# Performance work log

Hardware: AMD Instinct MI355X
Metric: run time of the kernel (lower is better)

## Reference

```python
import jax, jax.numpy as jnp
import numpy as np

DIM = 1024
NUM_HEADS = 16
SEQ_LEN = 4096


def setup_inputs() -> dict:
    key = jax.random.key(0)
    ks = jax.random.split(key, 9)
    s = DIM ** -0.5  # typical init scale for weights
    return {
        "x": jax.random.normal(ks[0], (SEQ_LEN, DIM), dtype=jnp.float32),
        "Wq": jax.random.normal(ks[1], (DIM, DIM), dtype=jnp.float32) * s,
        "bq": jax.random.normal(ks[2], (DIM,), dtype=jnp.float32) * s,
        "Wk": jax.random.normal(ks[3], (DIM, DIM), dtype=jnp.float32) * s,
        "bk": jax.random.normal(ks[4], (DIM,), dtype=jnp.float32) * s,
        "Wv": jax.random.normal(ks[5], (DIM, DIM), dtype=jnp.float32) * s,
        "bv": jax.random.normal(ks[6], (DIM,), dtype=jnp.float32) * s,
        "Wp": jax.random.normal(ks[7], (DIM, DIM), dtype=jnp.float32) * s,
        "bp": jax.random.normal(ks[8], (DIM,), dtype=jnp.float32) * s,
    }


def reference(x, Wq, bq, Wk, bk, Wv, bv, Wp, bp):
    T, C = x.shape
    H = NUM_HEADS
    Dh = C // H
    # QKV projections (eqx.nn.Linear: y = W @ x + b, vmapped over tokens)
    q = (x @ Wq.T + bq).reshape(T, H, Dh).swapaxes(0, 1)  # [H, T, Dh]
    k = (x @ Wk.T + bk).reshape(T, H, Dh).swapaxes(0, 1)
    v = (x @ Wv.T + bv).reshape(T, H, Dh).swapaxes(0, 1)
    # NOTE: original scales by C**-0.5 (full dim), not head_dim**-0.5
    attn = jnp.einsum("htd,hsd->hts", q, k) * (C ** -0.5)  # [H, T, T]
    causal = jnp.tril(jnp.ones((T, T), dtype=bool))[None, :, :]
    attn = jnp.where(causal, attn, -jnp.inf)
    attn = jax.nn.softmax(attn, axis=-1)
    out = jnp.einsum("hts,hsd->htd", attn, v)  # [H, T, Dh]
    out = out.swapaxes(0, 1).reshape(T, C)
    return out @ Wp.T + bp
```

## Files before the change

kernel.cpp:

```cpp
#include <hip/hip_runtime.h>
#include <stdint.h>

typedef unsigned short u16;
typedef __bf16 bf16x8 __attribute__((ext_vector_type(8)));
typedef u16 u16x8 __attribute__((ext_vector_type(8)));
typedef u16 u16x4 __attribute__((ext_vector_type(4)));
typedef float f32x4 __attribute__((ext_vector_type(4)));
typedef float f32x16 __attribute__((ext_vector_type(16)));

#define SEQ 4096
#define CD 1024
#define NH 16
#define DHD 64

__device__ __forceinline__ u16 f2bf(float f) {
  union { float f; unsigned u; } v; v.f = f;
  unsigned r = v.u + 0x7fffu + ((v.u >> 16) & 1u);
  return (u16)(r >> 16);
}
__device__ __forceinline__ unsigned fbits(float f) {
  union { float f; unsigned u; } v; v.f = f; return v.u;
}

__device__ __forceinline__ void load_lds16(const u16* g, u16* l) {
  __builtin_amdgcn_global_load_lds((const __attribute__((address_space(1))) void*)g,
                                   (__attribute__((address_space(3))) void*)l, 16, 0, 0);
}

__global__ __launch_bounds__(256) void cvt_all(const float* __restrict__ x, const float* __restrict__ Wq,
                                               const float* __restrict__ Wk, const float* __restrict__ Wv,
                                               const float* __restrict__ Wp,
                                               u16* __restrict__ xb, u16* __restrict__ Wb, u16* __restrict__ Wpb) {
  int b = blockIdx.x;
  const float* src; u16* dst; int base;
  if (b < 2048)      { src = x;  dst = xb;             base = b; }
  else if (b < 2560) { src = Wq; dst = Wb;             base = b - 2048; }
  else if (b < 3072) { src = Wk; dst = Wb + CD * CD;   base = b - 2560; }
  else if (b < 3584) { src = Wv; dst = Wb + 2*CD*CD;   base = b - 3072; }
  else               { src = Wp; dst = Wpb;            base = b - 3584; }
  int i = (base * 256 + (int)threadIdx.x) * 8;
  float4 a = *(const float4*)(src + i);
  float4 c = *(const float4*)(src + i + 4);
  u16x8 o;
  o[0] = f2bf(a.x); o[1] = f2bf(a.y); o[2] = f2bf(a.z); o[3] = f2bf(a.w);
  o[4] = f2bf(c.x); o[5] = f2bf(c.y); o[6] = f2bf(c.z); o[7] = f2bf(c.w);
  *(u16x8*)(dst + i) = o;
}

template<int MODE>
__device__ __forceinline__ void gemm_core(const u16* __restrict__ A, const u16* __restrict__ Bw,
                                          const float* __restrict__ bias, void* __restrict__ outp,
                                          float oscale) {
  constexpr int K = CD, N = CD;
  __shared__ u16 As[128 * 32];
  __shared__ u16 Bs[128 * 32];
  const int tid = threadIdx.x;
  const int w = tid >> 6, L = tid & 63, q = L >> 4, ln = L & 15;
  const int rowA0 = blockIdx.y * 128, rowB0 = blockIdx.x * 128;
  const int wr = (w >> 1) * 64, wc = (w & 1) * 64;
  f32x4 acc[4][4] = {};
  for (int k0 = 0; k0 < K; k0 += 32) {
#pragma unroll
    for (int pass = 0; pass < 2; ++pass) {
      int off = pass * 4096 + tid * 16;
      int row = off >> 6;
      int cole = (off & 63) >> 1;
      load_lds16(A + (size_t)(rowA0 + row) * K + k0 + cole, As + pass * 2048 + w * 512);
      load_lds16(Bw + (size_t)(rowB0 + row) * K + k0 + cole, Bs + pass * 2048 + w * 512);
    }
    __syncthreads();
    bf16x8 af[4], bg[4];
#pragma unroll
    for (int i = 0; i < 4; ++i) af[i] = *(const bf16x8*)(As + (wr + i * 16 + ln) * 32 + q * 8);
#pragma unroll
    for (int i = 0; i < 4; ++i) bg[i] = *(const bf16x8*)(Bs + (wc + i * 16 + ln) * 32 + q * 8);
#pragma unroll
    for (int i = 0; i < 4; ++i)
#pragma unroll
      for (int j = 0; j < 4; ++j)
        acc[i][j] = __builtin_amdgcn_mfma_f32_16x16x32_bf16(af[i], bg[j], acc[i][j], 0, 0, 0);
    __syncthreads();
  }
#pragma unroll
  for (int i = 0; i < 4; ++i) {
#pragma unroll
    for (int j = 0; j < 4; ++j) {
      int col = rowB0 + wc + j * 16 + ln;
      float bb = bias[col];
#pragma unroll
      for (int r = 0; r < 4; ++r) {
        int row = rowA0 + wr + i * 16 + q * 4 + r;
        float v = (acc[i][j][r] + bb) * oscale;
        if (MODE == 0)      ((u16*)outp)[(size_t)row * N + col] = f2bf(v);
        else if (MODE == 1) ((u16*)outp)[(size_t)col * SEQ + row] = f2bf(v);
        else                ((float*)outp)[(size_t)row * N + col] = v;
      }
    }
  }
}

__global__ __launch_bounds__(256) void gemm_qkv(const u16* __restrict__ A, const u16* __restrict__ W3,
                                                const float* __restrict__ bq, const float* __restrict__ bk,
                                                const float* __restrict__ bv, u16* __restrict__ Qb,
                                                u16* __restrict__ Kb, u16* __restrict__ VTb) {
  int z = blockIdx.z;
  if (z == 0)      gemm_core<0>(A, W3,               bq, Qb,  0.03125f);
  else if (z == 1) gemm_core<0>(A, W3 + CD * CD,     bk, Kb,  1.0f);
  else             gemm_core<1>(A, W3 + 2 * CD * CD, bv, VTb, 1.0f);
}

__global__ __launch_bounds__(256) void gemm_proj(const u16* __restrict__ A, const u16* __restrict__ Bw,
                                                 const float* __restrict__ bias, float* __restrict__ out) {
  gemm_core<2>(A, Bw, bias, out, 1.0f);
}

__global__ __launch_bounds__(128) void attn_kernel(const u16* __restrict__ Q, const u16* __restrict__ Kg,
                                                   const u16* __restrict__ VTg, u16* __restrict__ O) {
  __shared__ u16 Ks[2][64 * 72];
  __shared__ u16 Vt[2][64 * 72];
  const int tid = threadIdx.x, w = tid >> 6, L = tid & 63;
  const int ln = L & 31, hh = L >> 5;
  const int b = blockIdx.x;
  const int qt = (SEQ / 64 - 1) - (b >> 4);
  const int h = b & 15;
  const int colH = h * DHD;
  const int qrow0 = qt * 64 + w * 32;
  bf16x8 qf[4];
#pragma unroll
  for (int kk = 0; kk < 4; ++kk)
    qf[kk] = *(const bf16x8*)(Q + (size_t)(qrow0 + ln) * CD + colH + kk * 16 + hh * 8);
  f32x16 oa[2] = {};
  float lsum = 0.f;
  const int srow = tid >> 3, sx = tid & 7;
  u16x8 kr[4], vr[4];
#pragma unroll
  for (int p = 0; p < 4; ++p) {
    kr[p] = *(const u16x8*)(Kg + (size_t)(p * 16 + srow) * CD + colH + sx * 8);
    vr[p] = *(const u16x8*)(VTg + (size_t)(colH + p * 16 + srow) * SEQ + sx * 8);
  }
  for (int jt = 0; jt <= qt; ++jt) {
    const int buf = jt & 1;
    u16* KsB = Ks[buf];
    u16* VtB = Vt[buf];
#pragma unroll
    for (int p = 0; p < 4; ++p) {
      *(u16x8*)(KsB + (p * 16 + srow) * 72 + sx * 8) = kr[p];
      *(u16x8*)(VtB + (p * 16 + srow) * 72 + sx * 8) = vr[p];
    }
    __syncthreads();
    if (jt < qt) {
      const size_t kb2 = (size_t)(jt + 1) * 64;
#pragma unroll
      for (int p = 0; p < 4; ++p) {
        kr[p] = *(const u16x8*)(Kg + (kb2 + p * 16 + srow) * CD + colH + sx * 8);
        vr[p] = *(const u16x8*)(VTg + (size_t)(colH + p * 16 + srow) * SEQ + kb2 + sx * 8);
      }
    }
    const bool diag = (jt == qt);
    unsigned pk[16];
#pragma unroll
    for (int nt = 0; nt < 2; ++nt) {
      f32x16 a = {};
#pragma unroll
      for (int kk = 0; kk < 4; ++kk) {
        bf16x8 kf = *(const bf16x8*)(KsB + (nt * 32 + ln) * 72 + kk * 16 + hh * 8);
        a = __builtin_amdgcn_mfma_f32_32x32x16_bf16(kf, qf[kk], a, 0, 0, 0);
      }
#pragma unroll
      for (int r = 0; r < 16; ++r) {
        float sv = a[r];
        if (diag) {
          const int key_l = nt * 32 + (r & 3) + 8 * (r >> 2) + 4 * hh;
          if (key_l > w * 32 + ln) sv = -1e30f;
        }
        float p = __expf(sv);
        lsum += p;
        a[r] = p;
      }
#pragma unroll
      for (int i = 0; i < 8; ++i)
        pk[nt * 8 + i] = __builtin_amdgcn_perm(fbits(a[2 * i + 1]), fbits(a[2 * i]), 0x07060302);
    }
#pragma unroll
    for (int b0 = 0; b0 < 16; b0 += 4) {
      asm("v_permlane32_swap_b32 %0, %1" : "+v"(pk[b0 + 0]), "+v"(pk[b0 + 2]));
      asm("v_permlane32_swap_b32 %0, %1" : "+v"(pk[b0 + 1]), "+v"(pk[b0 + 3]));
    }
#pragma unroll
    for (int g = 0; g < 2; ++g)
#pragma unroll
      for (int s = 0; s < 4; ++s) {
        bf16x8 vf = *(const bf16x8*)(VtB + (g * 32 + ln) * 72 + s * 16 + hh * 8);
        union { unsigned u[4]; bf16x8 v; } pf;
        pf.u[0] = pk[s * 4 + 0]; pf.u[1] = pk[s * 4 + 1];
        pf.u[2] = pk[s * 4 + 2]; pf.u[3] = pk[s * 4 + 3];
        oa[g] = __builtin_amdgcn_mfma_f32_32x32x16_bf16(vf, pf.v, oa[g], 0, 0, 0);
      }
  }
  lsum += __shfl_xor(lsum, 32, 64);
  const float inv = 1.0f / lsum;
#pragma unroll
  for (int g = 0; g < 2; ++g)
#pragma unroll
    for (int rg = 0; rg < 4; ++rg) {
      u16x4 ov;
#pragma unroll
      for (int i = 0; i < 4; ++i) ov[i] = f2bf(oa[g][rg * 4 + i] * inv);
      *(u16x4*)(O + (size_t)(qrow0 + ln) * CD + colH + g * 32 + 8 * rg + 4 * hh) = ov;
    }
}

extern "C" void kernel_launch(void* const* d_in, const int* in_sizes, int n_in,
                              void* d_out, int out_size, void* d_ws, size_t ws_size,
                              hipStream_t stream) {
  const float* x  = (const float*)d_in[0];
  const float* Wq = (const float*)d_in[1];
  const float* bq = (const float*)d_in[2];
  const float* Wk = (const float*)d_in[3];
  const float* bk = (const float*)d_in[4];
  const float* Wv = (const float*)d_in[5];
  const float* bv = (const float*)d_in[6];
  const float* Wp = (const float*)d_in[7];
  const float* bp = (const float*)d_in[8];

  char* ws = (char*)d_ws;
  u16* xb  = (u16*)(ws);
  u16* Wb  = (u16*)(ws + (8u << 20));
  u16* Wpb = (u16*)(ws + (14u << 20));
  u16* Qb  = (u16*)(ws + (16u << 20));
  u16* Kb  = (u16*)(ws + (24u << 20));
  u16* VTb = (u16*)(ws + (32u << 20));
  u16* Ab  = (u16*)(ws + (40u << 20));

  cvt_all<<<4096, 256, 0, stream>>>(x, Wq, Wk, Wv, Wp, xb, Wb, Wpb);
  gemm_qkv<<<dim3(CD / 128, SEQ / 128, 3), 256, 0, stream>>>(xb, Wb, bq, bk, bv, Qb, Kb, VTb);
  attn_kernel<<<(SEQ / 64) * NH, 128, 0, stream>>>(Qb, Kb, VTb, Ab);
  gemm_proj<<<dim3(CD / 128, SEQ / 128), 256, 0, stream>>>(Ab, Wpb, bp, (float*)d_out);
}
```

Baseline: 223.6 us.

## Split attention key range across two wave pairs and merge partial sums

The attention block grows from 128 to 256 threads. Two wave pairs each process half of the causal key tiles for the same 64 query rows, each with its own LDS buffer, and their partial outputs and row sums are merged through shared memory at the end. This shortens the serial loop for long rows and raises parallelism, at the cost of an extra LDS reduction and more sync points. It also folds log2(e) into the Q scale so the kernel can use a native exp2, adds s_setprio around the MFMA sections, and splits the row sum into four partial accumulators.

```diff
diff --git a/kernel.cpp b/kernel.cpp
--- a/kernel.cpp
+++ b/kernel.cpp
@@ -20,6 +20,13 @@
 }
 __device__ __forceinline__ unsigned fbits(float f) {
   union { float f; unsigned u; } v; v.f = f; return v.u;
+}
+__device__ __forceinline__ float fexp2(float x) {
+#if __has_builtin(__builtin_amdgcn_exp2f)
+  return __builtin_amdgcn_exp2f(x);
+#else
+  return exp2f(x);
+#endif
 }
 
 __device__ __forceinline__ void load_lds16(const u16* g, u16* l) {
@@ -104,7 +111,7 @@
                                                 const float* __restrict__ bv, u16* __restrict__ Qb,
                                                 u16* __restrict__ Kb, u16* __restrict__ VTb) {
   int z = blockIdx.z;
-  if (z == 0)      gemm_core<0>(A, W3,               bq, Qb,  0.03125f);
+  if (z == 0)      gemm_core<0>(A, W3,               bq, Qb,  0.0450842200f);
   else if (z == 1) gemm_core<0>(A, W3 + CD * CD,     bk, Kb,  1.0f);
   else             gemm_core<1>(A, W3 + 2 * CD * CD, bv, VTb, 1.0f);
 }
@@ -114,100 +121,138 @@
   gemm_core<2>(A, Bw, bias, out, 1.0f);
 }
 
-__global__ __launch_bounds__(128) void attn_kernel(const u16* __restrict__ Q, const u16* __restrict__ Kg,
-                                                   const u16* __restrict__ VTg, u16* __restrict__ O) {
+__global__ __launch_bounds__(256, 4) void attn_kernel(const u16* __restrict__ Q, const u16* __restrict__ Kg,
+                                                      const u16* __restrict__ VTg, u16* __restrict__ O) {
   __shared__ u16 Ks[2][64 * 72];
   __shared__ u16 Vt[2][64 * 72];
   const int tid = threadIdx.x, w = tid >> 6, L = tid & 63;
   const int ln = L & 31, hh = L >> 5;
+  const int p = w >> 1, sub = w & 1;
   const int b = blockIdx.x;
   const int qt = (SEQ / 64 - 1) - (b >> 4);
   const int h = b & 15;
   const int colH = h * DHD;
-  const int qrow0 = qt * 64 + w * 32;
+  const int qrow0 = qt * 64 + sub * 32;
+  const int nt0 = (qt + 2) >> 1;
+  int jt = p ? nt0 : 0;
+  const int jt_end = p ? (qt + 1) : nt0;
   bf16x8 qf[4];
 #pragma unroll
   for (int kk = 0; kk < 4; ++kk)
     qf[kk] = *(const bf16x8*)(Q + (size_t)(qrow0 + ln) * CD + colH + kk * 16 + hh * 8);
   f32x16 oa[2] = {};
-  float lsum = 0.f;
-  const int srow = tid >> 3, sx = tid & 7;
+  f32x4 lsv = {};
+  const int ptid = tid & 127;
+  const int srow = ptid >> 3, sx = ptid & 7;
+  u16* KsP = Ks[p];
+  u16* VtP = Vt[p];
   u16x8 kr[4], vr[4];
-#pragma unroll
-  for (int p = 0; p < 4; ++p) {
-    kr[p] = *(const u16x8*)(Kg + (size_t)(p * 16 + srow) * CD + colH + sx * 8);
-    vr[p] = *(const u16x8*)(VTg + (size_t)(colH + p * 16 + srow) * SEQ + sx * 8);
-  }
-  for (int jt = 0; jt <= qt; ++jt) {
-    const int buf = jt & 1;
-    u16* KsB = Ks[buf];
-    u16* VtB = Vt[buf];
-#pragma unroll
-    for (int p = 0; p < 4; ++p) {
-      *(u16x8*)(KsB + (p * 16 + srow) * 72 + sx * 8) = kr[p];
-      *(u16x8*)(VtB + (p * 16 + srow) * 72 + sx * 8) = vr[p];
-    }
-    __syncthreads();
-    if (jt < qt) {
+  bool active = jt < jt_end;
+  if (active) {
+#pragma unroll
+    for (int c = 0; c < 4; ++c) {
+      kr[c] = *(const u16x8*)(Kg + (size_t)(jt * 64 + c * 16 + srow) * CD + colH + sx * 8);
+      vr[c] = *(const u16x8*)(VTg + (size_t)(colH + c * 16 + srow) * SEQ + jt * 64 + sx * 8);
+    }
+  }
+  for (int i = 0; i < nt0; ++i) {
+    if (active) {
+#pragma unroll
+      for (int c = 0; c < 4; ++c) {
+        *(u16x8*)(KsP + (c * 16 + srow) * 72 + sx * 8) = kr[c];
+        *(u16x8*)(VtP + (c * 16 + srow) * 72 + sx * 8) = vr[c];
+      }
+    }
+    __syncthreads();
+    const bool hasnext = (jt + 1) < jt_end;
+    if (hasnext) {
       const size_t kb2 = (size_t)(jt + 1) * 64;
 #pragma unroll
-      for (int p = 0; p < 4; ++p) {
-        kr[p] = *(const u16x8*)(Kg + (kb2 + p * 16 + srow) * CD + colH + sx * 8);
-        vr[p] = *(const u16x8*)(VTg + (size_t)(colH + p * 16 + srow) * SEQ + kb2 + sx * 8);
-      }
-    }
-    const bool diag = (jt == qt);
-    unsigned pk[16];
-#pragma unroll
-    for (int nt = 0; nt < 2; ++nt) {
-      f32x16 a = {};
-#pragma unroll
-      for (int kk = 0; kk < 4; ++kk) {
-        bf16x8 kf = *(const bf16x8*)(KsB + (nt * 32 + ln) * 72 + kk * 16 + hh * 8);
-        a = __builtin_amdgcn_mfma_f32_32x32x16_bf16(kf, qf[kk], a, 0, 0, 0);
-      }
-#pragma unroll
-      for (int r = 0; r < 16; ++r) {
-        float sv = a[r];
-        if (diag) {
-          const int key_l = nt * 32 + (r & 3) + 8 * (r >> 2) + 4 * hh;
-          if (key_l > w * 32 + ln) sv = -1e30f;
+      for (int c = 0; c < 4; ++c) {
+        kr[c] = *(const u16x8*)(Kg + (kb2 + c * 16 + srow) * CD + colH + sx * 8);
+        vr[c] = *(const u16x8*)(VTg + (size_t)(colH + c * 16 + srow) * SEQ + kb2 + sx * 8);
+      }
+    }
+    if (active) {
+      const bool diag = (jt == qt);
+      unsigned pk[16];
+#pragma unroll
+      for (int nt = 0; nt < 2; ++nt) {
+        f32x16 a = {};
+        __builtin_amdgcn_s_setprio(1);
+#pragma unroll
+        for (int kk = 0; kk < 4; ++kk) {
+          bf16x8 kf = *(const bf16x8*)(KsP + (nt * 32 + ln) * 72 + kk * 16 + hh * 8);
+          a = __builtin_amdgcn_mfma_f32_32x32x16_bf16(kf, qf[kk], a, 0, 0, 0);
         }
-        float p = __expf(sv);
-        lsum += p;
-        a[r] = p;
-      }
-#pragma unroll
-      for (int i = 0; i < 8; ++i)
-        pk[nt * 8 + i] = __builtin_amdgcn_perm(fbits(a[2 * i + 1]), fbits(a[2 * i]), 0x07060302);
-    }
-#pragma unroll
-    for (int b0 = 0; b0 < 16; b0 += 4) {
-      asm("v_permlane32_swap_b32 %0, %1" : "+v"(pk[b0 + 0]), "+v"(pk[b0 + 2]));
-      asm("v_permlane32_swap_b32 %0, %1" : "+v"(pk[b0 + 1]), "+v"(pk[b0 + 3]));
-    }
+        __builtin_amdgcn_s_setprio(0);
+#pragma unroll
+        for (int r = 0; r < 16; ++r) {
+          float sv = a[r];
+          if (diag) {
+            const int key_l = nt * 32 + (r & 3) + 8 * (r >> 2) + 4 * hh;
+            if (key_l > sub * 32 + ln) sv = -1e30f;
+          }
+          float pe = fexp2(sv);
+          lsv[r & 3] += pe;
+          a[r] = pe;
+        }
+#pragma unroll
+        for (int i2 = 0; i2 < 8; ++i2)
+          pk[nt * 8 + i2] = __builtin_amdgcn_perm(fbits(a[2 * i2 + 1]), fbits(a[2 * i2]), 0x07060302);
+      }
+#pragma unroll
+      for (int b0 = 0; b0 < 16; b0 += 4) {
+        asm("v_permlane32_swap_b32 %0, %1" : "+v"(pk[b0 + 0]), "+v"(pk[b0 + 2]));
+        asm("v_permlane32_swap_b32 %0, %1" : "+v"(pk[b0 + 1]), "+v"(pk[b0 + 3]));
+      }
+      __builtin_amdgcn_s_setprio(1);
+#pragma unroll
+      for (int g = 0; g < 2; ++g)
+#pragma unroll
+        for (int s = 0; s < 4; ++s) {
+          bf16x8 vf = *(const bf16x8*)(VtP + (g * 32 + ln) * 72 + s * 16 + hh * 8);
+          union { unsigned u[4]; bf16x8 v; } pf;
+          pf.u[0] = pk[s * 4 + 0]; pf.u[1] = pk[s * 4 + 1];
+          pf.u[2] = pk[s * 4 + 2]; pf.u[3] = pk[s * 4 + 3];
+          oa[g] = __builtin_amdgcn_mfma_f32_32x32x16_bf16(vf, pf.v, oa[g], 0, 0, 0);
+        }
+      __builtin_amdgcn_s_setprio(0);
+    }
+    __syncthreads();
+    ++jt;
+    active = active && (jt < jt_end);
+  }
+  float lsum = (lsv[0] + lsv[1]) + (lsv[2] + lsv[3]);
+  float* red = (float*)Ks;
+  if (p == 1) {
+    float* dst = red + ptid * 33;
 #pragma unroll
     for (int g = 0; g < 2; ++g)
 #pragma unroll
-      for (int s = 0; s < 4; ++s) {
-        bf16x8 vf = *(const bf16x8*)(VtB + (g * 32 + ln) * 72 + s * 16 + hh * 8);
-        union { unsigned u[4]; bf16x8 v; } pf;
-        pf.u[0] = pk[s * 4 + 0]; pf.u[1] = pk[s * 4 + 1];
-        pf.u[2] = pk[s * 4 + 2]; pf.u[3] = pk[s * 4 + 3];
-        oa[g] = __builtin_amdgcn_mfma_f32_32x32x16_bf16(vf, pf.v, oa[g], 0, 0, 0);
-      }
-  }
-  lsum += __shfl_xor(lsum, 32, 64);
-  const float inv = 1.0f / lsum;
-#pragma unroll
-  for (int g = 0; g < 2; ++g)
-#pragma unroll
-    for (int rg = 0; rg < 4; ++rg) {
-      u16x4 ov;
-#pragma unroll
-      for (int i = 0; i < 4; ++i) ov[i] = f2bf(oa[g][rg * 4 + i] * inv);
-      *(u16x4*)(O + (size_t)(qrow0 + ln) * CD + colH + g * 32 + 8 * rg + 4 * hh) = ov;
-    }
+      for (int r = 0; r < 16; ++r) dst[g * 16 + r] = oa[g][r];
+    dst[32] = lsum;
+  }
+  __syncthreads();
+  if (p == 0) {
+    const float* src = red + ptid * 33;
+#pragma unroll
+    for (int g = 0; g < 2; ++g)
+#pragma unroll
+      for (int r = 0; r < 16; ++r) oa[g][r] += src[g * 16 + r];
+    lsum += src[32];
+    lsum += __shfl_xor(lsum, 32, 64);
+    const float inv = 1.0f / lsum;
+#pragma unroll
+    for (int g = 0; g < 2; ++g)
+#pragma unroll
+      for (int rg = 0; rg < 4; ++rg) {
+        u16x4 ov;
+#pragma unroll
+        for (int i2 = 0; i2 < 4; ++i2) ov[i2] = f2bf(oa[g][rg * 4 + i2] * inv);
+        *(u16x4*)(O + (size_t)(qrow0 + ln) * CD + colH + g * 32 + 8 * rg + 4 * hh) = ov;
+      }
+  }
 }
 
 extern "C" void kernel_launch(void* const* d_in, const int* in_sizes, int n_in,
@@ -234,6 +279,6 @@
 
   cvt_all<<<4096, 256, 0, stream>>>(x, Wq, Wk, Wv, Wp, xb, Wb, Wpb);
   gemm_qkv<<<dim3(CD / 128, SEQ / 128, 3), 256, 0, stream>>>(xb, Wb, bq, bk, bv, Qb, Kb, VTb);
-  attn_kernel<<<(SEQ / 64) * NH, 128, 0, stream>>>(Qb, Kb, VTb, Ab);
+  attn_kernel<<<(SEQ / 64) * NH, 256, 0, stream>>>(Qb, Kb, VTb, Ab);
   gemm_proj<<<dim3(CD / 128, SEQ / 128), 256, 0, stream>>>(Ab, Wpb, bp, (float*)d_out);
 }
```

Result: slower. 274.4 us (+22.7%).
